# Optimization experiments

Hardware: AMD Instinct MI355X
Metric: run time of the kernel (lower is better)

## Reference

```python
import jax, jax.numpy as jnp
import numpy as np

N = 16384      # number of nodes
U = 128        # feature units
AVG_DEGREE = 32


def setup_inputs() -> dict:
    key = jax.random.key(0)
    kx, ka, kw = jax.random.split(key, 3)
    x = jax.random.normal(kx, (N, U), dtype=jnp.float32)
    # Sparse binary adjacency (avg degree ~32), stored dense because the
    # original module densifies it via tf.sparse.to_dense before matmul.
    adj = (jax.random.uniform(ka, (N, N)) < (AVG_DEGREE / N)).astype(jnp.float32)
    W = jax.random.normal(kw, (U, U), dtype=jnp.float32) * 0.05  # 'random_normal' init
    b = jnp.zeros((U,), dtype=jnp.float32)
    return {"x": x, "adj": adj, "W": W, "b": b}


def reference(x, adj, W, b):
    adj = jax.lax.stop_gradient(adj)
    # hop 1: aggregate neighbors, dense linear, swish
    neigh1 = adj @ x                      # [N, U]
    x1 = jax.nn.swish(neigh1 @ W + b)     # [N, U]
    # hop 2: same weights W, b (shared across both hops in the original)
    neigh2 = adj @ x1                     # [N, U]
    x2 = jax.nn.swish(neigh2 @ W + b)     # [N, U]
    return x2
```

## Files before the change

### kernel.cpp

```cpp
#include <hip/hip_runtime.h>
#include <stdint.h>

#define NN 16384
#define UU 128
#define CAP 128
#define LCAP 8

typedef unsigned short u16;
typedef unsigned int uv4 __attribute__((ext_vector_type(4)));

__device__ __forceinline__ float4 gather_row_sum(const float* __restrict__ src,
                                                 const u16* sIdx, int c,
                                                 int half, int sl) {
    float4 acc = {0.f, 0.f, 0.f, 0.f};
#pragma unroll 8
    for (int k = half; k < c; k += 2) {
        const int j = sIdx[k];
        const float4 v = *reinterpret_cast<const float4*>(src + (size_t)j * UU + sl * 4);
        acc.x += v.x; acc.y += v.y; acc.z += v.z; acc.w += v.w;
    }
    acc.x += __shfl_xor(acc.x, 32);
    acc.y += __shfl_xor(acc.y, 32);
    acc.z += __shfl_xor(acc.z, 32);
    acc.w += __shfl_xor(acc.w, 32);
    return acc;
}

__device__ __forceinline__ void block_linear_swish(const float (*sNeigh)[UU],
                                                   const float* __restrict__ W,
                                                   const float* __restrict__ bias,
                                                   float* __restrict__ dst,
                                                   int rowBase, int tid) {
    const int u = tid & 127;
    const int g = tid >> 7;
    const float bu = bias[u];
    float f0 = bu, f1 = bu;
    for (int v = 0; v < UU; ++v) {
        const float w = W[v * UU + u];
        f0 += sNeigh[2 * g + 0][v] * w;
        f1 += sNeigh[2 * g + 1][v] * w;
    }
    const float s0 = f0 / (1.0f + __expf(-f0));
    const float s1 = f1 / (1.0f + __expf(-f1));
    dst[(size_t)(rowBase + 2 * g + 0) * UU + u] = s0;
    dst[(size_t)(rowBase + 2 * g + 1) * UU + u] = s1;
}

__global__ __launch_bounds__(256) void fused_sparsify_hop1(
    const float* __restrict__ adj, const float* __restrict__ x,
    const float* __restrict__ W, const float* __restrict__ bias,
    float* __restrict__ x1, u16* __restrict__ ell, unsigned* __restrict__ cnt) {
    __shared__ u16   raw[4][64 * LCAP];
    __shared__ u16   sIdx[4][CAP];
    __shared__ float sNeigh[4][UU];

    const int tid  = threadIdx.x;
    const int wave = tid >> 6;
    const int lane = tid & 63;
    const int rowBase = blockIdx.x * 4;
    const int row  = rowBase + wave;

    const uv4* rowp = reinterpret_cast<const uv4*>(adj + (size_t)row * NN);
    u16* myraw = &raw[wave][lane * LCAP];
    int myCnt = 0;
    for (int it = 0; it < NN / 256; ++it) {
        const uv4 v = __builtin_nontemporal_load(&rowp[it * 64 + lane]);
        const unsigned col0 = (unsigned)((it * 64 + lane) * 4);
        const unsigned vals[4] = {v.x, v.y, v.z, v.w};
#pragma unroll
        for (int e = 0; e < 4; ++e) {
            if (vals[e] != 0u) {
                if (myCnt < LCAP) myraw[myCnt] = (u16)(col0 + e);
                ++myCnt;
            }
        }
    }
    if (myCnt > LCAP) myCnt = LCAP;

    int pre = myCnt;
#pragma unroll
    for (int d = 1; d < 64; d <<= 1) {
        int t = __shfl_up(pre, d);
        if (lane >= d) pre += t;
    }
    const int excl  = pre - myCnt;
    const int total = __shfl(pre, 63);
    const int c = (total < CAP) ? total : CAP;
    if (lane == 0) cnt[row] = (unsigned)c;

    for (int i = 0; i < myCnt; ++i) {
        const int pos = excl + i;
        if (pos < CAP) sIdx[wave][pos] = myraw[i];
    }

    for (int p = lane; p < c; p += 64) ell[(size_t)row * CAP + p] = sIdx[wave][p];

    const int half = lane >> 5;
    const int sl   = lane & 31;
    float4 acc = gather_row_sum(x, sIdx[wave], c, half, sl);
    if (half == 0) *reinterpret_cast<float4*>(&sNeigh[wave][sl * 4]) = acc;
    __syncthreads();

    block_linear_swish(sNeigh, W, bias, x1, rowBase, tid);
}

__global__ __launch_bounds__(256) void fused_hop2(
    const float* __restrict__ x1, const u16* __restrict__ ell,
    const unsigned* __restrict__ cnt, const float* __restrict__ W,
    const float* __restrict__ bias, float* __restrict__ out) {
    __shared__ u16   sIdx[4][CAP];
    __shared__ float sNeigh[4][UU];

    const int tid  = threadIdx.x;
    const int wave = tid >> 6;
    const int lane = tid & 63;
    const int rowBase = blockIdx.x * 4;
    const int row  = rowBase + wave;

    const int c = (int)cnt[row];
    const ushort2* ellRow = reinterpret_cast<const ushort2*>(ell + (size_t)row * CAP);
    reinterpret_cast<ushort2*>(sIdx[wave])[lane] = ellRow[lane];

    const int half = lane >> 5;
    const int sl   = lane & 31;
    float4 acc = gather_row_sum(x1, sIdx[wave], c, half, sl);
    if (half == 0) *reinterpret_cast<float4*>(&sNeigh[wave][sl * 4]) = acc;
    __syncthreads();

    block_linear_swish(sNeigh, W, bias, out, rowBase, tid);
}

extern "C" void kernel_launch(void* const* d_in, const int* in_sizes, int n_in,
                              void* d_out, int out_size, void* d_ws, size_t ws_size,
                              hipStream_t stream) {
    const float* x   = (const float*)d_in[0];
    const float* adj = (const float*)d_in[1];
    const float* W   = (const float*)d_in[2];
    const float* b   = (const float*)d_in[3];
    float* out = (float*)d_out;

    char* ws = (char*)d_ws;
    float*    x1  = (float*)(ws);
    u16*      ell = (u16*)  (ws + (size_t)8 * 1024 * 1024);
    unsigned* cnt = (unsigned*)(ws + (size_t)12 * 1024 * 1024);

    fused_sparsify_hop1<<<NN / 4, 256, 0, stream>>>(adj, x, W, b, x1, ell, cnt);
    fused_hop2<<<NN / 4, 256, 0, stream>>>(x1, ell, cnt, W, b, out);
}
```

Measured before the change: 243.8 us.

## Store hop-1 activations in bf16 and software-pipeline adjacency row scan

The intermediate x1 is now written as bf16 and hop 2 gathers bf16 rows with 16 lanes per row and 4 rows in flight, which halves gather traffic for the second hop. The adjacency scan in hop 1 is restructured to prefetch the next batch of four 16-byte loads while scanning the current batch, to raise memory-level parallelism. The cost is reduced precision in the intermediate activations and higher register pressure in the scan loop. The dominant cost is still streaming the 1 GiB dense adjacency.

Measured after the change: 221.9 us. 9.0% less time.

```diff
diff --git a/kernel.cpp b/kernel.cpp
--- a/kernel.cpp
+++ b/kernel.cpp
@@ -1,4 +1,5 @@
 #include <hip/hip_runtime.h>
+#include <hip/hip_bf16.h>
 #include <stdint.h>
 
 #define NN 16384
@@ -9,9 +10,9 @@
 typedef unsigned short u16;
 typedef unsigned int uv4 __attribute__((ext_vector_type(4)));
 
-__device__ __forceinline__ float4 gather_row_sum(const float* __restrict__ src,
-                                                 const u16* sIdx, int c,
-                                                 int half, int sl) {
+__device__ __forceinline__ float4 gather_row_sum_f32(const float* __restrict__ src,
+                                                     const u16* sIdx, int c,
+                                                     int half, int sl) {
     float4 acc = {0.f, 0.f, 0.f, 0.f};
 #pragma unroll 8
     for (int k = half; k < c; k += 2) {
@@ -26,10 +27,11 @@
     return acc;
 }
 
+template <typename OutT>
 __device__ __forceinline__ void block_linear_swish(const float (*sNeigh)[UU],
                                                    const float* __restrict__ W,
                                                    const float* __restrict__ bias,
-                                                   float* __restrict__ dst,
+                                                   OutT* __restrict__ dst,
                                                    int rowBase, int tid) {
     const int u = tid & 127;
     const int g = tid >> 7;
@@ -42,14 +44,22 @@
     }
     const float s0 = f0 / (1.0f + __expf(-f0));
     const float s1 = f1 / (1.0f + __expf(-f1));
-    dst[(size_t)(rowBase + 2 * g + 0) * UU + u] = s0;
-    dst[(size_t)(rowBase + 2 * g + 1) * UU + u] = s1;
+    const size_t i0 = (size_t)(rowBase + 2 * g + 0) * UU + u;
+    const size_t i1 = (size_t)(rowBase + 2 * g + 1) * UU + u;
+    if constexpr (sizeof(OutT) == 2) {
+        dst[i0] = __float2bfloat16(s0);
+        dst[i1] = __float2bfloat16(s1);
+    } else {
+        dst[i0] = s0;
+        dst[i1] = s1;
+    }
 }
 
 __global__ __launch_bounds__(256) void fused_sparsify_hop1(
     const float* __restrict__ adj, const float* __restrict__ x,
     const float* __restrict__ W, const float* __restrict__ bias,
-    float* __restrict__ x1, u16* __restrict__ ell, unsigned* __restrict__ cnt) {
+    __hip_bfloat16* __restrict__ x1, u16* __restrict__ ell,
+    unsigned* __restrict__ cnt) {
     __shared__ u16   raw[4][64 * LCAP];
     __shared__ u16   sIdx[4][CAP];
     __shared__ float sNeigh[4][UU];
@@ -63,17 +73,35 @@
     const uv4* rowp = reinterpret_cast<const uv4*>(adj + (size_t)row * NN);
     u16* myraw = &raw[wave][lane * LCAP];
     int myCnt = 0;
-    for (int it = 0; it < NN / 256; ++it) {
-        const uv4 v = __builtin_nontemporal_load(&rowp[it * 64 + lane]);
-        const unsigned col0 = (unsigned)((it * 64 + lane) * 4);
-        const unsigned vals[4] = {v.x, v.y, v.z, v.w};
+
+    uv4 c0 = __builtin_nontemporal_load(&rowp[0 * 64 + lane]);
+    uv4 c1 = __builtin_nontemporal_load(&rowp[1 * 64 + lane]);
+    uv4 c2 = __builtin_nontemporal_load(&rowp[2 * 64 + lane]);
+    uv4 c3 = __builtin_nontemporal_load(&rowp[3 * 64 + lane]);
+
+    for (int b = 0; b < 16; ++b) {
+        uv4 n0 = c0, n1 = c1, n2 = c2, n3 = c3;
+        if (b < 15) {
+            const uv4* nb = rowp + (size_t)(b + 1) * 256 + lane;
+            n0 = __builtin_nontemporal_load(nb + 0 * 64);
+            n1 = __builtin_nontemporal_load(nb + 1 * 64);
+            n2 = __builtin_nontemporal_load(nb + 2 * 64);
+            n3 = __builtin_nontemporal_load(nb + 3 * 64);
+        }
+        const uv4 vv[4] = {c0, c1, c2, c3};
 #pragma unroll
-        for (int e = 0; e < 4; ++e) {
-            if (vals[e] != 0u) {
-                if (myCnt < LCAP) myraw[myCnt] = (u16)(col0 + e);
-                ++myCnt;
+        for (int j = 0; j < 4; ++j) {
+            const unsigned colBase = (unsigned)(((b * 4 + j) * 64 + lane) * 4);
+            const unsigned vals[4] = {vv[j].x, vv[j].y, vv[j].z, vv[j].w};
+#pragma unroll
+            for (int e = 0; e < 4; ++e) {
+                if (vals[e] != 0u) {
+                    if (myCnt < LCAP) myraw[myCnt] = (u16)(colBase + e);
+                    ++myCnt;
+                }
             }
         }
+        c0 = n0; c1 = n1; c2 = n2; c3 = n3;
     }
     if (myCnt > LCAP) myCnt = LCAP;
 
@@ -97,7 +125,7 @@
 
     const int half = lane >> 5;
     const int sl   = lane & 31;
-    float4 acc = gather_row_sum(x, sIdx[wave], c, half, sl);
+    float4 acc = gather_row_sum_f32(x, sIdx[wave], c, half, sl);
     if (half == 0) *reinterpret_cast<float4*>(&sNeigh[wave][sl * 4]) = acc;
     __syncthreads();
 
@@ -105,7 +133,7 @@
 }
 
 __global__ __launch_bounds__(256) void fused_hop2(
-    const float* __restrict__ x1, const u16* __restrict__ ell,
+    const __hip_bfloat16* __restrict__ x1, const u16* __restrict__ ell,
     const unsigned* __restrict__ cnt, const float* __restrict__ W,
     const float* __restrict__ bias, float* __restrict__ out) {
     __shared__ u16   sIdx[4][CAP];
@@ -121,10 +149,32 @@
     const ushort2* ellRow = reinterpret_cast<const ushort2*>(ell + (size_t)row * CAP);
     reinterpret_cast<ushort2*>(sIdx[wave])[lane] = ellRow[lane];
 
-    const int half = lane >> 5;
-    const int sl   = lane & 31;
-    float4 acc = gather_row_sum(x1, sIdx[wave], c, half, sl);
-    if (half == 0) *reinterpret_cast<float4*>(&sNeigh[wave][sl * 4]) = acc;
+    const int q = lane >> 4;
+    const int s = lane & 15;
+    float a[8] = {0.f, 0.f, 0.f, 0.f, 0.f, 0.f, 0.f, 0.f};
+#pragma unroll 4
+    for (int k = q; k < c; k += 4) {
+        const int j = sIdx[wave][k];
+        const uv4 v = *reinterpret_cast<const uv4*>(
+            reinterpret_cast<const u16*>(x1) + (size_t)j * UU + s * 8);
+        const unsigned d[4] = {v.x, v.y, v.z, v.w};
+#pragma unroll
+        for (int m = 0; m < 4; ++m) {
+            a[2 * m]     += __uint_as_float(d[m] << 16);
+            a[2 * m + 1] += __uint_as_float(d[m] & 0xffff0000u);
+        }
+    }
+#pragma unroll
+    for (int m = 0; m < 8; ++m) {
+        a[m] += __shfl_xor(a[m], 16);
+        a[m] += __shfl_xor(a[m], 32);
+    }
+    if (q == 0) {
+        float4 lo = {a[0], a[1], a[2], a[3]};
+        float4 hi = {a[4], a[5], a[6], a[7]};
+        *reinterpret_cast<float4*>(&sNeigh[wave][s * 8])     = lo;
+        *reinterpret_cast<float4*>(&sNeigh[wave][s * 8 + 4]) = hi;
+    }
     __syncthreads();
 
     block_linear_swish(sNeigh, W, bias, out, rowBase, tid);
@@ -140,9 +190,9 @@
     float* out = (float*)d_out;
 
     char* ws = (char*)d_ws;
-    float*    x1  = (float*)(ws);
-    u16*      ell = (u16*)  (ws + (size_t)8 * 1024 * 1024);
-    unsigned* cnt = (unsigned*)(ws + (size_t)12 * 1024 * 1024);
+    __hip_bfloat16* x1  = (__hip_bfloat16*)(ws);
+    u16*            ell = (u16*)(ws + (size_t)4 * 1024 * 1024);
+    unsigned*       cnt = (unsigned*)(ws + (size_t)8 * 1024 * 1024);
 
     fused_sparsify_hop1<<<NN / 4, 256, 0, stream>>>(adj, x, W, b, x1, ell, cnt);
     fused_hop2<<<NN / 4, 256, 0, stream>>>(x1, ell, cnt, W, b, out);
```
